# Performance work log

Hardware: AMD Instinct MI355X
Metric: run time of the kernel (lower is better)

## Reference

```python
import jax, jax.numpy as jnp
import numpy as np

# Static config (matches init_kwargs)
B = 1
D = 1024          # model_dim
H = 16            # num_heads
HD = 64           # head_dim
TPF = 256         # tokens_per_frame = latent_height*latent_width
LH, LW = 16, 16
FRAMES = 13
PREFIX = 1
ATTN = 3
CHUNKS = 4
TXT = 226                 # text_length per chunk
SEQ_TXT = CHUNKS * TXT    # 904
VID_LEN = FRAMES * TPF    # 3328
CHUNK_VID = (PREFIX + ATTN) * TPF  # 1024 video tokens per attention chunk
THETA = 10000.0
EPS = 1e-6
SCALE = 1.0 / np.sqrt(HD)
DT, DHE, DW = 16, 24, 24  # 3D rope split of head_dim


def setup_inputs() -> dict:
    key = jax.random.key(0)
    ks = jax.random.split(key, 16)
    def w(k, shape, s=0.02):
        return (jax.random.normal(k, shape) * s).astype(jnp.float32)
    return dict(
        vid_emb=jax.random.normal(ks[0], (B, VID_LEN, D), jnp.float32),
        text_emb=jax.random.normal(ks[1], (B, SEQ_TXT, D), jnp.float32),
        Wq=w(ks[2], (D, D)), bq=jnp.zeros((D,), jnp.float32),
        Wk=w(ks[3], (D, D)), bk=jnp.zeros((D,), jnp.float32),
        Wv=w(ks[4], (D, D)), bv=jnp.zeros((D,), jnp.float32),
        Wo=w(ks[5], (D, D)), bo=jnp.zeros((D,), jnp.float32),
        qn_w=jnp.ones((HD,), jnp.float32), qn_b=jnp.zeros((HD,), jnp.float32),
        kn_w=jnp.ones((HD,), jnp.float32), kn_b=jnp.zeros((HD,), jnp.float32),
        ssm_Win=w(ks[6], (D, D)), ssm_Wout=w(ks[7], (D, D)),
        ssm_gate=jnp.zeros((D,), jnp.float32),
        fg_t=jnp.full((D,), 0.1, jnp.float32), fg_v=jnp.full((D,), 0.1, jnp.float32),
        bg_t=jnp.full((D,), 0.1, jnp.float32), bg_v=jnp.full((D,), 0.1, jnp.float32),
    )


def _layernorm(x, w, b):
    mu = jnp.mean(x, axis=-1, keepdims=True)
    var = jnp.mean((x - mu) ** 2, axis=-1, keepdims=True)
    return (x - mu) * jax.lax.rsqrt(var + EPS) * w + b


def _rope_angles():
    # per-video-token 3D positions within a chunk
    tok = jnp.arange(CHUNK_VID)
    f = (tok // TPF).astype(jnp.float32)
    rem = tok % TPF
    hp = (rem // LW).astype(jnp.float32)
    wp = (rem % LW).astype(jnp.float32)
    def inv(d):
        return THETA ** (-jnp.arange(0, d, 2, dtype=jnp.float32) / d)
    return f[:, None] * inv(DT), hp[:, None] * inv(DHE), wp[:, None] * inv(DW)


def _rot(x, ang):
    half = x.shape[-1] // 2
    c, s = jnp.cos(ang), jnp.sin(ang)
    x1, x2 = x[..., :half], x[..., half:]
    return jnp.concatenate([x1 * c - x2 * s, x1 * s + x2 * c], axis=-1)


def _apply_rope3d(x, angs):
    at, ah, aw = angs
    return jnp.concatenate([
        _rot(x[..., :DT], at),
        _rot(x[..., DT:DT + DHE], ah),
        _rot(x[..., DT + DHE:], aw),
    ], axis=-1)


def _attn_forward(vid_emb, text_emb, Wq, bq, Wk, bk, Wv, bv, Wo, bo, qn_w, qn_b, kn_w, kn_b):
    b = vid_emb.shape[0]
    starts = np.arange(CHUNKS) * ATTN * TPF
    idx = jnp.asarray(starts)[:, None] + jnp.arange(CHUNK_VID)[None, :]  # [C, CHUNK_VID]
    txt_chunks = text_emb.reshape(b, CHUNKS, TXT, D)
    vid_chunks = vid_emb[:, idx]                                          # [b, C, CHUNK_VID, D]
    cur = jnp.concatenate([txt_chunks, vid_chunks], axis=2)               # [b, C, T, D]
    T = TXT + CHUNK_VID
    cur = cur.reshape(b * CHUNKS, T, D)

    def heads(x):
        return x.reshape(b * CHUNKS, T, H, HD).transpose(0, 2, 1, 3)      # [bc, h, t, d]

    q = _layernorm(heads(cur @ Wq + bq), qn_w, qn_b)
    k = _layernorm(heads(cur @ Wk + bk), kn_w, kn_b)
    v = heads(cur @ Wv + bv)

    angs = _rope_angles()
    q = jnp.concatenate([q[:, :, :TXT], _apply_rope3d(q[:, :, TXT:], angs)], axis=2)
    k = jnp.concatenate([k[:, :, :TXT], _apply_rope3d(k[:, :, TXT:], angs)], axis=2)

    scores = jnp.einsum('bhqd,bhkd->bhqk', q, k) * SCALE
    attn = jax.nn.softmax(scores, axis=-1)
    out = jnp.einsum('bhqk,bhkd->bhqd', attn, v)
    out = out.transpose(0, 2, 1, 3).reshape(b * CHUNKS, T, D) @ Wo + bo
    out = out.reshape(b, CHUNKS, T, D)

    text_out = out[:, :, :TXT].reshape(b, SEQ_TXT, D)
    vid_part = out[:, :, TXT:]                                            # [b, C, CHUNK_VID, D]
    vid_acc = jnp.zeros((b, VID_LEN, D), vid_emb.dtype).at[:, idx].add(vid_part)
    cnt = jnp.zeros((b, VID_LEN, 1), vid_emb.dtype).at[:, idx].add(jnp.ones((b, CHUNKS, CHUNK_VID, 1), vid_emb.dtype))
    vid_out = vid_acc / cnt
    return jnp.concatenate([text_out, vid_out], axis=1)


def _ssm(x, Win, Wout, gate_logit):
    # simplified TTT stand-in: gated linear recurrence h_t = g*h_{t-1} + u_t (causal scan)
    g = jax.nn.sigmoid(gate_logit)
    u = x @ Win
    a = jnp.broadcast_to(g, u.shape)
    def comb(c1, c2):
        a1, b1 = c1
        a2, b2 = c2
        return a1 * a2, a2 * b1 + b2
    _, h = jax.lax.associative_scan(comb, (a, u), axis=1)
    return h @ Wout


def _rev_text_chunks(t):
    b = t.shape[0]
    return jnp.flip(t.reshape(b, CHUNKS, TXT, D), axis=1).reshape(b, SEQ_TXT, D)


def _ssm_forward(emb, ssm_Win, ssm_Wout, ssm_gate, fg_t, fg_v, bg_t, bg_v):
    Ttxt = SEQ_TXT
    res = emb
    y = _ssm(emb, ssm_Win, ssm_Wout, ssm_gate)
    emb = res + jnp.concatenate([jnp.tanh(fg_t) * y[:, :Ttxt], jnp.tanh(fg_v) * y[:, Ttxt:]], axis=1)
    res2 = emb
    # multiscene reverse: flip text chunk order and video token order
    rev = jnp.concatenate([_rev_text_chunks(emb[:, :Ttxt]), jnp.flip(emb[:, Ttxt:], axis=1)], axis=1)
    y2 = _ssm(rev, ssm_Win, ssm_Wout, ssm_gate)
    y2 = jnp.concatenate([_rev_text_chunks(y2[:, :Ttxt]), jnp.flip(y2[:, Ttxt:], axis=1)], axis=1)
    return res2 + jnp.concatenate([jnp.tanh(bg_t) * y2[:, :Ttxt], jnp.tanh(bg_v) * y2[:, Ttxt:]], axis=1)


def reference(vid_emb, text_emb, Wq, bq, Wk, bk, Wv, bv, Wo, bo, qn_w, qn_b, kn_w, kn_b,
              ssm_Win, ssm_Wout, ssm_gate, fg_t, fg_v, bg_t, bg_v):
    emb = _attn_forward(vid_emb, text_emb, Wq, bq, Wk, bk, Wv, bv, Wo, bo, qn_w, qn_b, kn_w, kn_b)
    out = _ssm_forward(emb, ssm_Win, ssm_Wout, ssm_gate, fg_t, fg_v, bg_t, bg_v)
    return out[:, SEQ_TXT:], out[:, :SEQ_TXT]
```

## Files before the change

### kernel.cpp

```cpp
#include <hip/hip_runtime.h>
#include <cstdint>

constexpr int Dm       = 1024;
constexpr int Hh       = 16;
constexpr int HD       = 64;
constexpr int CHUNKS   = 4;
constexpr int TXT      = 226;
constexpr int SEQ_TXT  = 904;
constexpr int VID_LEN  = 3328;
constexpr int CHUNK_VID= 1024;
constexpr int Tt       = 1250;
constexpr int Tp       = 1280;
constexpr int M_QKV    = 5000;
constexpr int SEQm     = 4232;
constexpr int STRIDE_V = 768;
constexpr float EPSc   = 1e-6f;
constexpr float SCALEc = 0.125f;
constexpr float OFFS   = 8.0f;
constexpr float C16    = 1.6609640474f;
constexpr float C24    = 1.1073093649f;

constexpr int SEGL2 = 64;
constexpr int HALO  = 64;
constexpr int NSEG2 = (SEQm + SEGL2 - 1) / SEGL2;

typedef __attribute__((ext_vector_type(8))) short bf16x8;
typedef __attribute__((ext_vector_type(4))) float f32x4;

__device__ __forceinline__ ushort f2bf(float x) {
    uint32_t u = __float_as_uint(x);
    u += 0x7FFFu + ((u >> 16) & 1u);
    return (ushort)(u >> 16);
}
__device__ __forceinline__ float bf2f(ushort b) {
    return __uint_as_float(((uint32_t)b) << 16);
}

__device__ __forceinline__ void gload_lds16(const ushort* g, ushort* l) {
    __builtin_amdgcn_global_load_lds(
        (const __attribute__((address_space(1))) unsigned int*)g,
        (__attribute__((address_space(3))) unsigned int*)l, 16, 0, 0);
}

__device__ __forceinline__ int rev_map(int i) {
    if (i < SEQ_TXT) {
        int c = i / TXT, o = i - c * TXT;
        return (CHUNKS - 1 - c) * TXT + o;
    }
    int j = i - SEQ_TXT;
    return SEQ_TXT + (VID_LEN - 1 - j);
}

__global__ __launch_bounds__(256) void prep_all(
    const float* __restrict__ Wq, const float* __restrict__ Wk,
    const float* __restrict__ Wv, const float* __restrict__ Wo,
    const float* __restrict__ Win, const float* __restrict__ Wout,
    const float* __restrict__ vid, const float* __restrict__ txt,
    ushort* __restrict__ WqkvH, ushort* __restrict__ WqkvL,
    ushort* __restrict__ WoH, ushort* __restrict__ WoL,
    ushort* __restrict__ WinH, ushort* __restrict__ WinL,
    ushort* __restrict__ WoutH, ushort* __restrict__ WoutL,
    ushort* __restrict__ chi, ushort* __restrict__ clo) {
    __shared__ float tile[32][33];
    if (blockIdx.z == 6) {
        int base = (blockIdx.y * 32 + blockIdx.x) * 256 + threadIdx.x;
        for (int idx = base; idx < M_QKV * 256; idx += 32 * 32 * 256) {
            int row = idx >> 8, c4 = (idx & 255) * 4;
            int c = row / Tt, t = row - c * Tt;
            float4 x;
            if (t < TXT)
                x = *(const float4*)(txt + (size_t)(c * TXT + t) * Dm + c4);
            else
                x = *(const float4*)(vid + (size_t)(c * STRIDE_V + (t - TXT)) * Dm + c4);
            float v[4] = {x.x, x.y, x.z, x.w};
            ushort4 h, l;
            h.x = f2bf(v[0]); l.x = f2bf(v[0] - bf2f(h.x));
            h.y = f2bf(v[1]); l.y = f2bf(v[1] - bf2f(h.y));
            h.z = f2bf(v[2]); l.z = f2bf(v[2] - bf2f(h.z));
            h.w = f2bf(v[3]); l.w = f2bf(v[3] - bf2f(h.w));
            *(ushort4*)(chi + (size_t)row * Dm + c4) = h;
            *(ushort4*)(clo + (size_t)row * Dm + c4) = l;
        }
        return;
    }
    const float* W; ushort* Thi; ushort* Tlo;
    switch (blockIdx.z) {
        case 0: W = Wq;  Thi = WqkvH;               Tlo = WqkvL;               break;
        case 1: W = Wk;  Thi = WqkvH + 1024*1024;   Tlo = WqkvL + 1024*1024;   break;
        case 2: W = Wv;  Thi = WqkvH + 2*1024*1024; Tlo = WqkvL + 2*1024*1024; break;
        case 3: W = Wo;  Thi = WoH;   Tlo = WoL;   break;
        case 4: W = Win; Thi = WinH;  Tlo = WinL;  break;
        default:W = Wout;Thi = WoutH; Tlo = WoutL; break;
    }
    int k0 = blockIdx.y * 32, n0 = blockIdx.x * 32;
    int j = threadIdx.x & 31, i0 = threadIdx.x >> 5;
#pragma unroll
    for (int i = i0; i < 32; i += 8)
        tile[i][j] = W[(size_t)(k0 + i) * 1024 + n0 + j];
    __syncthreads();
#pragma unroll
    for (int i = i0; i < 32; i += 8) {
        float v = tile[j][i];
        ushort h = f2bf(v);
        size_t o = (size_t)(n0 + i) * 1024 + k0 + j;
        Thi[o] = h;
        Tlo[o] = f2bf(v - bf2f(h));
    }
}

template<int MODE>
__global__ __launch_bounds__(256) void gemm_sk(
    const ushort* __restrict__ Ahi, const ushort* __restrict__ Alo,
    const ushort* __restrict__ Bhi, const ushort* __restrict__ Blo,
    const float* __restrict__ f1, const float* __restrict__ f2,
    const float* __restrict__ f3,
    float* __restrict__ Cf, ushort* __restrict__ u1,
    int M, int N) {
    __shared__ ushort AHL[2][128 * 64];
    __shared__ ushort BHL[2][128 * 64];
    const int tid = threadIdx.x;
    const int w = tid >> 6, lane = tid & 63;
    const int lrow = lane & 15, quad = lane >> 4;
    const int mBase = blockIdx.y * 128, nBase = blockIdx.x * 128;

    const bool isB = (w >= 2);
    const int half = w & 1;
    const ushort* Phi = isB ? Bhi : Ahi;
    const ushort* Plo = isB ? Blo : Alo;
    ushort* st0 = (isB ? BHL[0] : AHL[0]) + half * 4096;
    ushort* st1 = (isB ? BHL[1] : AHL[1]) + half * 4096;
    const int baseR = (isB ? nBase : mBase) + half * 64;
    const int maxr = (isB ? N : M) - 1;
    const int rl8 = lane >> 3;
    const int c = (lane & 7) ^ rl8;
    const ushort* Psel = (c < 4) ? Phi : Plo;
    const ushort* gb[8];
#pragma unroll
    for (int u = 0; u < 8; ++u) {
        int rg = min(baseR + u * 8 + rl8, maxr);
        gb[u] = Psel + (size_t)rg * 1024 + (c & 3) * 8;
    }

    const int mo = (w >> 1) * 64, no = (w & 1) * 64;
    const int p = quad ^ (lrow & 7);
    f32x4 acc[4][4];
#pragma unroll
    for (int i = 0; i < 4; ++i)
#pragma unroll
        for (int j = 0; j < 4; ++j) acc[i][j] = (f32x4){0.f, 0.f, 0.f, 0.f};

    const int kk0 = (MODE == 5) ? blockIdx.z * 512 : 0;
    const int kk1 = (MODE == 5) ? kk0 + 512 : 1024;

#pragma unroll
    for (int u = 0; u < 8; ++u) gload_lds16(gb[u] + kk0, st0 + u * 512);
    asm volatile("s_waitcnt vmcnt(0)" ::: "memory");
    __builtin_amdgcn_s_barrier();

    int it = 0;
    for (int kk = kk0; kk < kk1; kk += 32, ++it) {
        const int b = it & 1;
        ushort* stN = b ? st0 : st1;
        if (kk + 32 < kk1) {
#pragma unroll
            for (int u = 0; u < 8; ++u) gload_lds16(gb[u] + kk + 32, stN + u * 512);
        }

        const ushort* Ab = AHL[b];
        const ushort* Bb = BHL[b];
        bf16x8 ah[4], al[4], bh[4], bl[4];
#pragma unroll
        for (int i = 0; i < 4; ++i) {
            int m = mo + i * 16 + lrow;
            ah[i] = *(const bf16x8*)&Ab[m * 64 + p * 8];
            al[i] = *(const bf16x8*)&Ab[m * 64 + (p ^ 4) * 8];
        }
#pragma unroll
        for (int j = 0; j < 4; ++j) {
            int n = no + j * 16 + lrow;
            bh[j] = *(const bf16x8*)&Bb[n * 64 + p * 8];
            bl[j] = *(const bf16x8*)&Bb[n * 64 + (p ^ 4) * 8];
        }
        __builtin_amdgcn_s_setprio(1);
#pragma unroll
        for (int i = 0; i < 4; ++i)
#pragma unroll
            for (int j = 0; j < 4; ++j) {
                f32x4 a = acc[i][j];
                a = __builtin_amdgcn_mfma_f32_16x16x32_bf16(ah[i], bh[j], a, 0, 0, 0);
                a = __builtin_amdgcn_mfma_f32_16x16x32_bf16(al[i], bh[j], a, 0, 0, 0);
                a = __builtin_amdgcn_mfma_f32_16x16x32_bf16(ah[i], bl[j], a, 0, 0, 0);
                acc[i][j] = a;
            }
        __builtin_amdgcn_s_setprio(0);
        asm volatile("s_waitcnt vmcnt(0)" ::: "memory");
        __builtin_amdgcn_s_barrier();
    }

    const size_t zoff = (MODE == 5) ? (size_t)blockIdx.z * M * N : 0;
#pragma unroll
    for (int i = 0; i < 4; ++i)
#pragma unroll
        for (int j = 0; j < 4; ++j) {
            const int col = nBase + no + j * 16 + lrow;
            float bv = 0.f;
            if constexpr (MODE == 1)
                bv = (col < 1024) ? f1[col]
                   : (col < 2048) ? f2[col - 1024] : f3[col - 2048];
#pragma unroll
            for (int r = 0; r < 4; ++r) {
                const int row = mBase + mo + i * 16 + quad * 4 + r;
                if (row >= M) continue;
                const size_t idx = (size_t)row * N + col;
                const float a = acc[i][j][r];
                if constexpr (MODE == 1) {
                    u1[idx] = f2bf(a + bv);
                } else {
                    Cf[zoff + idx] = a;
                }
            }
        }
}

__global__ __launch_bounds__(512, 2) void gemm_qkv_8ph(
    const ushort* __restrict__ Ahi, const ushort* __restrict__ Alo,
    const ushort* __restrict__ Bhi, const ushort* __restrict__ Blo,
    const float* __restrict__ f1, const float* __restrict__ f2,
    const float* __restrict__ f3, ushort* __restrict__ out) {
    constexpr int Mq  = M_QKV;
    constexpr int Nq  = 3072;
    constexpr int NSL = 32;

    __shared__ __align__(16) ushort ldsq[65536];

    const int tid = threadIdx.x;
    const int w = tid >> 6, lane = tid & 63;
    const int lrow = lane & 15, quad = lane >> 4;
    const int wr = w >> 2, wc = w & 3;
    const int mBase = blockIdx.y * 256, nBase = blockIdx.x * 256;

    const int cA = (tid & 7) ^ ((tid >> 3) & 7);
    const ushort* pA = (cA < 4) ? Ahi : Alo;
    const ushort* pB = (cA < 4) ? Bhi : Blo;
    uint32_t offA[4], offB[4];
#pragma unroll
    for (int q = 0; q < 4; ++q) {
        const int r = q * 64 + (tid >> 3);
        offA[q] = (uint32_t)(min(mBase + r, Mq - 1) * 1024 + (cA & 3) * 8);
        offB[q] = (uint32_t)((nBase + r) * 1024 + (cA & 3) * 8);
    }
    const int ldsW = w * 512;

    const int pH = quad ^ (lrow & 7);
    const int arow = wr * 128 + lrow;
    const int brow = wc * 64 + lrow;

    f32x4 acc[8][4];
#pragma unroll
    for (int i = 0; i < 8; ++i)
#pragma unroll
        for (int j = 0; j < 4; ++j) acc[i][j] = (f32x4){0.f, 0.f, 0.f, 0.f};

#define STAGE_AB(b, s) do { \
        ushort* dA_ = ldsq + (b) * 16384 + ldsW; \
        ushort* dB_ = ldsq + 32768 + (b) * 16384 + ldsW; \
        const uint32_t ko_ = (uint32_t)(s) * 32u; \
        gload_lds16(pA + offA[0] + ko_, dA_); \
        gload_lds16(pA + offA[1] + ko_, dA_ + 4096); \
        gload_lds16(pA + offA[2] + ko_, dA_ + 8192); \
        gload_lds16(pA + offA[3] + ko_, dA_ + 12288); \
        gload_lds16(pB + offB[0] + ko_, dB_); \
        gload_lds16(pB + offB[1] + ko_, dB_ + 4096); \
        gload_lds16(pB + offB[2] + ko_, dB_ + 8192); \
        gload_lds16(pB + offB[3] + ko_, dB_ + 12288); \
    } while (0)

    STAGE_AB(0, 0);
    asm volatile("s_waitcnt vmcnt(0)" ::: "memory");
    __builtin_amdgcn_s_barrier();

#pragma unroll 1
    for (int s = 0; s < NSL; ++s) {
        const int b = s & 1;
        if (s + 1 < NSL) STAGE_AB(1 - b, s + 1);

        const ushort* aB_ = ldsq + b * 16384;
        const ushort* bB_ = ldsq + 32768 + b * 16384;
        bf16x8 ahi[8], alo[8], bhi[4], blo[4];
#pragma unroll
        for (int i = 0; i < 8; ++i) {
            const ushort* rp = aB_ + (arow + i * 16) * 64;
            ahi[i] = *(const bf16x8*)(rp + pH * 8);
            alo[i] = *(const bf16x8*)(rp + (pH ^ 4) * 8);
        }
#pragma unroll
        for (int j = 0; j < 4; ++j) {
            const ushort* rp = bB_ + (brow + j * 16) * 64;
            bhi[j] = *(const bf16x8*)(rp + pH * 8);
            blo[j] = *(const bf16x8*)(rp + (pH ^ 4) * 8);
        }

        __builtin_amdgcn_s_barrier();
        asm volatile("s_waitcnt lgkmcnt(0)" ::: "memory");
        __builtin_amdgcn_s_setprio(1);
#pragma unroll
        for (int i = 0; i < 8; ++i)
#pragma unroll
            for (int j = 0; j < 4; ++j) {
                f32x4 a = acc[i][j];
                a = __builtin_amdgcn_mfma_f32_16x16x32_bf16(ahi[i], bhi[j], a, 0, 0, 0);
                a = __builtin_amdgcn_mfma_f32_16x16x32_bf16(alo[i], bhi[j], a, 0, 0, 0);
                a = __builtin_amdgcn_mfma_f32_16x16x32_bf16(ahi[i], blo[j], a, 0, 0, 0);
                acc[i][j] = a;
            }
        __builtin_amdgcn_s_setprio(0);
        asm volatile("s_waitcnt vmcnt(0)" ::: "memory");
        __builtin_amdgcn_s_barrier();
    }

#undef STAGE_AB

#pragma unroll
    for (int i = 0; i < 8; ++i) {
#pragma unroll
        for (int j = 0; j < 4; ++j) {
            const int col = nBase + wc * 64 + j * 16 + lrow;
            const float bias = (col < 1024) ? f1[col]
                             : (col < 2048) ? f2[col - 1024] : f3[col - 2048];
#pragma unroll
            for (int r = 0; r < 4; ++r) {
                const int row = mBase + wr * 128 + i * 16 + quad * 4 + r;
                if (row < Mq)
                    out[(size_t)row * Nq + col] = f2bf(acc[i][j][r] + bias);
            }
        }
    }
}

__global__ __launch_bounds__(256) void lnrope(
    const ushort* __restrict__ qkvb,
    const float* __restrict__ qn_w, const float* __restrict__ qn_b,
    const float* __restrict__ kn_w, const float* __restrict__ kn_b,
    ushort* __restrict__ qP, ushort* __restrict__ kP, ushort* __restrict__ vT) {
    __shared__ ushort vtile[64][72];
    const int ch = blockIdx.y, c = ch >> 4, h = ch & 15;
    const int t0 = blockIdx.x * 64;
    const int tid = threadIdx.x, w = tid >> 6, lane = tid & 63;

    auto wsum = [](float x) {
#pragma unroll
        for (int o = 32; o; o >>= 1) x += __shfl_xor(x, o);
        return x;
    };

#pragma unroll 1
    for (int it = 0; it < 16; ++it) {
        const int tl = w * 16 + it;
        const int t = t0 + tl;
        ushort qb = 0, kb = 0, vb = 0;
        if (t < Tt) {
            size_t src = (size_t)(c * Tt + t) * 3072 + h * HD + lane;
            float qv = bf2f(qkvb[src]);
            float kv = bf2f(qkvb[src + 1024]);
            float vv = bf2f(qkvb[src + 2048]);

            float qmu = wsum(qv) * (1.f / 64.f);
            float qd  = qv - qmu;
            float qvar = wsum(qd * qd) * (1.f / 64.f);
            float qn = qd * rsqrtf(qvar + EPSc) * qn_w[lane] + qn_b[lane];

            float kmu = wsum(kv) * (1.f / 64.f);
            float kd  = kv - kmu;
            float kvar = wsum(kd * kd) * (1.f / 64.f);
            float kn = kd * rsqrtf(kvar + EPSc) * kn_w[lane] + kn_b[lane];

            if (t >= TXT) {
                int pos = t - TXT;
                int f = pos >> 8, rem2 = pos & 255, hp = rem2 >> 4, wp = rem2 & 15;
                int p, dl; float cc;
                if (lane < 16)      { cc = C16; p = f;  dl = lane; }
                else if (lane < 40) { cc = C24; p = hp; dl = lane - 16; }
                else                { cc = C24; p = wp; dl = lane - 40; }
                int halfd = (lane < 16) ? 8 : 12;
                int i = (dl < halfd) ? dl : dl - halfd;
                float ang = (float)p * exp2f(-(float)i * cc);
                float cs = cosf(ang), sn = sinf(ang);
                int partner = (dl < halfd) ? (lane + halfd) : (lane - halfd);
                float qo = __shfl(qn, partner);
                float ko = __shfl(kn, partner);
                qn = (dl < halfd) ? (qn * cs - qo * sn) : (qo * sn + qn * cs);
                kn = (dl < halfd) ? (kn * cs - ko * sn) : (ko * sn + kn * cs);
            }
            qb = f2bf(qn * SCALEc);
            kb = f2bf(kn);
            vb = f2bf(vv);
        }
        size_t dst = ((size_t)ch * Tp + t) * HD + lane;
        qP[dst] = qb;
        kP[dst] = kb;
        vtile[tl][lane] = vb;
    }
    __syncthreads();
    const int r = tid >> 2, ck = tid & 3;
    ushort* dst = vT + ((size_t)ch * HD + r) * Tp + t0;
    short o1[8], o2[8];
#pragma unroll
    for (int j = 0; j < 8; ++j) {
        o1[j] = (short)vtile[ck * 8 + j][r];
        o2[j] = (short)vtile[(ck + 4) * 8 + j][r];
    }
    *(bf16x8*)(dst + ck * 8)       = *(bf16x8*)o1;
    *(bf16x8*)(dst + (ck + 4) * 8) = *(bf16x8*)o2;
}

__global__ __launch_bounds__(256) void attn_mfma(
    const ushort* __restrict__ qP, const ushort* __restrict__ kP,
    const ushort* __restrict__ vT,
    ushort* __restrict__ ohi, ushort* __restrict__ olo) {
    const int ch = blockIdx.y;
    const int c = ch >> 4, h = ch & 15;
    const int qbase = blockIdx.x * 64;
    const int tid = threadIdx.x, w = tid >> 6, lane = tid & 63;
    const int lrow = lane & 15, quad = lane >> 4;

    __shared__ ushort KT[2][32 * 64];
    __shared__ ushort VTs[2][64 * 32];
    __shared__ ushort PB[4][16][40];

    const ushort* kg = kP + (size_t)ch * Tp * HD;
    const ushort* vg = vT + (size_t)ch * HD * Tp;

    const ushort* kgl = kg + (size_t)(w * 8 + (lane >> 3)) * HD
                           + ((lane & 7) ^ ((lane >> 3) & 7)) * 8;
    const ushort* vgl = vg + (size_t)(w * 16 + (lane >> 2)) * Tp + (lane & 3) * 8;

    const int qr = qbase + w * 16 + lrow;
    const ushort* qgp = qP + ((size_t)ch * Tp + qr) * HD + quad * 8;
    bf16x8 qf0 = *(const bf16x8*)qgp;
    bf16x8 qf1 = *(const bf16x8*)(qgp + 32);

    f32x4 accO[4];
#pragma unroll
    for (int dt = 0; dt < 4; ++dt) accO[dt] = (f32x4){0.f, 0.f, 0.f, 0.f};
    float lacc[4] = {0.f, 0.f, 0.f, 0.f};

    gload_lds16(kgl, &KT[0][w * 512]);
    gload_lds16(vgl, &VTs[0][w * 512]);

    const int NSTEP = Tp / 32;
    for (int s = 0; s < NSTEP; ++s) {
        const int b = s & 1;
        __syncthreads();
        if (s + 1 < NSTEP) {
            int kb = (s + 1) * 32;
            gload_lds16(kgl + (size_t)kb * HD, &KT[1 - b][w * 512]);
            gload_lds16(vgl + kb, &VTs[1 - b][w * 512]);
        }

        const int sw = lrow & 7;
        const ushort* r0 = &KT[b][lrow * 64];
        const ushort* r1 = &KT[b][(16 + lrow) * 64];
        bf16x8 k00 = *(const bf16x8*)(r0 + (quad ^ sw) * 8);
        bf16x8 k01 = *(const bf16x8*)(r0 + ((4 + quad) ^ sw) * 8);
        bf16x8 k10 = *(const bf16x8*)(r1 + (quad ^ sw) * 8);
        bf16x8 k11 = *(const bf16x8*)(r1 + ((4 + quad) ^ sw) * 8);
        f32x4 s0 = (f32x4){0.f, 0.f, 0.f, 0.f}, s1 = s0;
        s0 = __builtin_amdgcn_mfma_f32_16x16x32_bf16(qf0, k00, s0, 0, 0, 0);
        s0 = __builtin_amdgcn_mfma_f32_16x16x32_bf16(qf1, k01, s0, 0, 0, 0);
        s1 = __builtin_amdgcn_mfma_f32_16x16x32_bf16(qf0, k10, s1, 0, 0, 0);
        s1 = __builtin_amdgcn_mfma_f32_16x16x32_bf16(qf1, k11, s1, 0, 0, 0);

#pragma unroll
        for (int r = 0; r < 4; ++r) {
            float p0 = __expf(s0[r] - OFFS);
            float p1 = __expf(s1[r] - OFFS);
            lacc[r] += p0 + p1;
            int row = quad * 4 + r;
            PB[w][row][lrow]      = f2bf(p0);
            PB[w][row][16 + lrow] = f2bf(p1);
        }

        bf16x8 pf = *(const bf16x8*)&PB[w][lrow][quad * 8];
#pragma unroll
        for (int dt = 0; dt < 4; ++dt) {
            bf16x8 vf = *(const bf16x8*)&VTs[b][(dt * 16 + lrow) * 32 + quad * 8];
            accO[dt] = __builtin_amdgcn_mfma_f32_16x16x32_bf16(pf, vf, accO[dt], 0, 0, 0);
        }
    }

    float il[4];
#pragma unroll
    for (int r = 0; r < 4; ++r) {
        float l = lacc[r];
        l += __shfl_xor(l, 1);
        l += __shfl_xor(l, 2);
        l += __shfl_xor(l, 4);
        l += __shfl_xor(l, 8);
        l -= (float)(Tp - Tt) * __expf(-OFFS);
        il[r] = 1.f / l;
    }
#pragma unroll
    for (int dt = 0; dt < 4; ++dt)
#pragma unroll
        for (int r = 0; r < 4; ++r) {
            int qrow = qbase + w * 16 + quad * 4 + r;
            if (qrow < Tt) {
                float val = accO[dt][r] * il[r];
                size_t o = (size_t)(c * Tt + qrow) * Dm + h * HD + dt * 16 + lrow;
                ushort hv = f2bf(val);
                ohi[o] = hv;
                olo[o] = f2bf(val - bf2f(hv));
            }
        }
}

__global__ __launch_bounds__(256) void reduce_scatter(
    const float* __restrict__ P0, const float* __restrict__ bo,
    ushort* __restrict__ ehi, ushort* __restrict__ elo) {
    const float* P1 = P0 + (size_t)M_QKV * Dm;
    int idx = blockIdx.x * 256 + threadIdx.x;
    int row = idx >> 8, c4 = (idx & 255) * 4;
    float sx, sy, sz, sw;
    if (row < SEQ_TXT) {
        int c = row / TXT, t = row - c * TXT;
        size_t o = (size_t)(c * Tt + t) * Dm + c4;
        float4 a = *(const float4*)(P0 + o);
        float4 b = *(const float4*)(P1 + o);
        sx = a.x + b.x; sy = a.y + b.y; sz = a.z + b.z; sw = a.w + b.w;
    } else {
        int p = row - SEQ_TXT;
        sx = sy = sz = sw = 0.f; int cnt = 0;
#pragma unroll
        for (int c = 0; c < CHUNKS; ++c) {
            int off = p - c * STRIDE_V;
            if (off >= 0 && off < CHUNK_VID) {
                size_t o = (size_t)(c * Tt + TXT + off) * Dm + c4;
                float4 a = *(const float4*)(P0 + o);
                float4 b = *(const float4*)(P1 + o);
                sx += a.x + b.x; sy += a.y + b.y;
                sz += a.z + b.z; sw += a.w + b.w;
                ++cnt;
            }
        }
        float inv = 1.f / (float)cnt;
        sx *= inv; sy *= inv; sz *= inv; sw *= inv;
    }
    float4 b4 = *(const float4*)(bo + c4);
    float v[4] = {sx + b4.x, sy + b4.y, sz + b4.z, sw + b4.w};
    ushort4 h, l;
    h.x = f2bf(v[0]); l.x = f2bf(v[0] - bf2f(h.x));
    h.y = f2bf(v[1]); l.y = f2bf(v[1] - bf2f(h.y));
    h.z = f2bf(v[2]); l.z = f2bf(v[2] - bf2f(h.z));
    h.w = f2bf(v[3]); l.w = f2bf(v[3] - bf2f(h.w));
    *(ushort4*)(ehi + (size_t)row * Dm + c4) = h;
    *(ushort4*)(elo + (size_t)row * Dm + c4) = l;
}

__global__ __launch_bounds__(256) void scan_halo(
    const float* __restrict__ P0, const float* __restrict__ gate,
    ushort* __restrict__ hhi, ushort* __restrict__ hlo, int perm) {
    const float* P1 = P0 + (size_t)SEQm * Dm;
    int ch = blockIdx.x * 256 + threadIdx.x;
    int seg = blockIdx.y;
    float g = 1.f / (1.f + expf(-gate[ch]));
    int tw0 = seg * SEGL2;
    int tw1 = min(SEQm, tw0 + SEGL2);
    int t0 = max(0, tw0 - HALO);
    float hv = 0.f;
    for (int t = t0; t < tw0; ++t) {
        int rt = perm ? rev_map(t) : t;
        size_t o = (size_t)rt * Dm + ch;
        hv = fmaf(g, hv, P0[o] + P1[o]);
    }
    for (int t = tw0; t < tw1; ++t) {
        int rt = perm ? rev_map(t) : t;
        size_t o = (size_t)rt * Dm + ch;
        hv = fmaf(g, hv, P0[o] + P1[o]);
        ushort h = f2bf(hv);
        hhi[o] = h;
        hlo[o] = f2bf(hv - bf2f(h));
    }
}

__global__ __launch_bounds__(256) void reduce_c1(
    const float* __restrict__ P0,
    const ushort* __restrict__ ehi, const ushort* __restrict__ elo,
    const float* __restrict__ fg_t, const float* __restrict__ fg_v,
    float* __restrict__ emb2, ushort* __restrict__ e2hi, ushort* __restrict__ e2lo) {
    const float* P1 = P0 + (size_t)SEQm * Dm;
    int idx = blockIdx.x * 256 + threadIdx.x;
    int row = idx >> 8, c4 = (idx & 255) * 4;
    const float* fg = (row < SEQ_TXT) ? fg_t : fg_v;
    size_t o = (size_t)row * Dm + c4;
    float4 a = *(const float4*)(P0 + o);
    float4 b = *(const float4*)(P1 + o);
    ushort4 eh = *(const ushort4*)(ehi + o);
    ushort4 el = *(const ushort4*)(elo + o);
    float v[4];
    v[0] = (bf2f(eh.x) + bf2f(el.x)) + tanhf(fg[c4 + 0]) * (a.x + b.x);
    v[1] = (bf2f(eh.y) + bf2f(el.y)) + tanhf(fg[c4 + 1]) * (a.y + b.y);
    v[2] = (bf2f(eh.z) + bf2f(el.z)) + tanhf(fg[c4 + 2]) * (a.z + b.z);
    v[3] = (bf2f(eh.w) + bf2f(el.w)) + tanhf(fg[c4 + 3]) * (a.w + b.w);
    *(float4*)(emb2 + o) = make_float4(v[0], v[1], v[2], v[3]);
    ushort4 h, l;
    h.x = f2bf(v[0]); l.x = f2bf(v[0] - bf2f(h.x));
    h.y = f2bf(v[1]); l.y = f2bf(v[1] - bf2f(h.y));
    h.z = f2bf(v[2]); l.z = f2bf(v[2] - bf2f(h.z));
    h.w = f2bf(v[3]); l.w = f2bf(v[3] - bf2f(h.w));
    *(ushort4*)(e2hi + o) = h;
    *(ushort4*)(e2lo + o) = l;
}

__global__ __launch_bounds__(256) void reduce_fin(
    const float* __restrict__ P0, const float* __restrict__ emb2,
    const float* __restrict__ bg_t, const float* __restrict__ bg_v,
    float* __restrict__ outp) {
    const float* P1 = P0 + (size_t)SEQm * Dm;
    int idx = blockIdx.x * 256 + threadIdx.x;
    int row = idx >> 8, c4 = (idx & 255) * 4;
    const float* bg = (row < SEQ_TXT) ? bg_t : bg_v;
    int drow = (row >= SEQ_TXT) ? (row - SEQ_TXT) : (VID_LEN + row);
    size_t o = (size_t)row * Dm + c4;
    float4 a = *(const float4*)(P0 + o);
    float4 b = *(const float4*)(P1 + o);
    float4 e = *(const float4*)(emb2 + o);
    float4 r = make_float4(e.x + tanhf(bg[c4 + 0]) * (a.x + b.x),
                           e.y + tanhf(bg[c4 + 1]) * (a.y + b.y),
                           e.z + tanhf(bg[c4 + 2]) * (a.z + b.z),
                           e.w + tanhf(bg[c4 + 3]) * (a.w + b.w));
    *(float4*)(outp + (size_t)drow * Dm + c4) = r;
}

extern "C" void kernel_launch(void* const* d_in, const int* in_sizes, int n_in,
                              void* d_out, int out_size, void* d_ws, size_t ws_size,
                              hipStream_t stream) {
    const float* vid_emb = (const float*)d_in[0];
    const float* text_emb= (const float*)d_in[1];
    const float* Wq = (const float*)d_in[2];  const float* bq = (const float*)d_in[3];
    const float* Wk = (const float*)d_in[4];  const float* bk = (const float*)d_in[5];
    const float* Wv = (const float*)d_in[6];  const float* bv = (const float*)d_in[7];
    const float* Wo = (const float*)d_in[8];  const float* bo = (const float*)d_in[9];
    const float* qn_w = (const float*)d_in[10]; const float* qn_b = (const float*)d_in[11];
    const float* kn_w = (const float*)d_in[12]; const float* kn_b = (const float*)d_in[13];
    const float* Win  = (const float*)d_in[14]; const float* Wout = (const float*)d_in[15];
    const float* gate = (const float*)d_in[16];
    const float* fg_t = (const float*)d_in[17]; const float* fg_v = (const float*)d_in[18];
    const float* bg_t = (const float*)d_in[19]; const float* bg_v = (const float*)d_in[20];

    char* W8 = (char*)d_ws;
    if (ws_size < 128647168u) return;
    ushort* WqkvH = (ushort*)(W8 + 0);
    ushort* WqkvL = (ushort*)(W8 + 6291456);
    ushort* WoH   = (ushort*)(W8 + 12582912);
    ushort* WoL   = (ushort*)(W8 + 14680064);
    ushort* WinH  = (ushort*)(W8 + 16777216);
    ushort* WinL  = (ushort*)(W8 + 18874368);
    ushort* WoutH = (ushort*)(W8 + 20971520);
    ushort* WoutL = (ushort*)(W8 + 23068672);
    ushort* qkvb  = (ushort*)(W8 + 25165824);
    ushort* curH  = (ushort*)(W8 + 55885824);
    ushort* curL  = (ushort*)(W8 + 66125824);
    ushort* qPl   = (ushort*)(W8 + 76365824);
    ushort* kPl   = (ushort*)(W8 + 86851584);
    ushort* vTl   = (ushort*)(W8 + 97337344);
    ushort* aoutH = (ushort*)(W8 + 25165824);
    ushort* aoutL = (ushort*)(W8 + 35405824);
    float*  PWo   = (float*) (W8 + 76365824);
    ushort* embH  = (ushort*)(W8 + 45645824);
    ushort* embL  = (ushort*)(W8 + 54312960);
    float*  PW    = (float*) (W8 + 76365824);
    ushort* hbufH = (ushort*)(W8 + 25165824);
    ushort* hbufL = (ushort*)(W8 + 33832960);
    float*  emb2  = (float*) (W8 + 111034368);
    ushort* e2H   = (ushort*)(W8 + 25165824);
    ushort* e2L   = (ushort*)(W8 + 33832960);
    ushort* hbuf2H= (ushort*)(W8 + 45645824);
    ushort* hbuf2L= (ushort*)(W8 + 54312960);
    float*  outp  = (float*)d_out;

    prep_all<<<dim3(32, 32, 7), 256, 0, stream>>>(
        Wq, Wk, Wv, Wo, Win, Wout, vid_emb, text_emb,
        WqkvH, WqkvL, WoH, WoL, WinH, WinL, WoutH, WoutL, curH, curL);

    gemm_qkv_8ph<<<dim3(12, 20), 512, 0, stream>>>(
        curH, curL, WqkvH, WqkvL, bq, bk, bv, qkvb);

    lnrope<<<dim3(Tp / 64, 64), 256, 0, stream>>>(qkvb, qn_w, qn_b, kn_w, kn_b,
                                                  qPl, kPl, vTl);

    attn_mfma<<<dim3(Tp / 64, 64), 256, 0, stream>>>(qPl, kPl, vTl, aoutH, aoutL);

    gemm_sk<5><<<dim3(8, 40, 2), 256, 0, stream>>>(
        aoutH, aoutL, WoH, WoL, nullptr, nullptr, nullptr, PWo, nullptr,
        M_QKV, 1024);
    reduce_scatter<<<SEQm, 256, 0, stream>>>(PWo, bo, embH, embL);

    dim3 gsq(8, 34, 2);
    dim3 gscan(Dm / 256, NSEG2);

    gemm_sk<5><<<gsq, 256, 0, stream>>>(
        embH, embL, WinH, WinL, nullptr, nullptr, nullptr, PW, nullptr,
        SEQm, 1024);
    scan_halo<<<gscan, 256, 0, stream>>>(PW, gate, hbufH, hbufL, 0);
    gemm_sk<5><<<gsq, 256, 0, stream>>>(
        hbufH, hbufL, WoutH, WoutL, nullptr, nullptr, nullptr, PW, nullptr,
        SEQm, 1024);
    reduce_c1<<<SEQm, 256, 0, stream>>>(PW, embH, embL, fg_t, fg_v,
                                        emb2, e2H, e2L);

    gemm_sk<5><<<gsq, 256, 0, stream>>>(
        e2H, e2L, WinH, WinL, nullptr, nullptr, nullptr, PW, nullptr,
        SEQm, 1024);
    scan_halo<<<gscan, 256, 0, stream>>>(PW, gate, hbuf2H, hbuf2L, 1);
    gemm_sk<5><<<gsq, 256, 0, stream>>>(
        hbuf2H, hbuf2L, WoutH, WoutL, nullptr, nullptr, nullptr, PW, nullptr,
        SEQm, 1024);
    reduce_fin<<<SEQm, 256, 0, stream>>>(PW, emb2, bg_t, bg_v, outp);
}
```

Baseline: 647.2 us.

## Replace split-K GEMM with full-K 128x64 tile GEMM and drop partial sums

Result: no change. 647.7 us (median of 2 runs) (+0.1%).

```diff
diff --git a/kernel.cpp b/kernel.cpp
--- a/kernel.cpp
+++ b/kernel.cpp
@@ -108,84 +108,77 @@
     }
 }
 
-template<int MODE>
-__global__ __launch_bounds__(256) void gemm_sk(
+__global__ __launch_bounds__(256) void gemm_fk(
     const ushort* __restrict__ Ahi, const ushort* __restrict__ Alo,
     const ushort* __restrict__ Bhi, const ushort* __restrict__ Blo,
-    const float* __restrict__ f1, const float* __restrict__ f2,
-    const float* __restrict__ f3,
-    float* __restrict__ Cf, ushort* __restrict__ u1,
-    int M, int N) {
+    float* __restrict__ Cf, int M, int N) {
     __shared__ ushort AHL[2][128 * 64];
-    __shared__ ushort BHL[2][128 * 64];
+    __shared__ ushort BHL[2][64 * 64];
     const int tid = threadIdx.x;
     const int w = tid >> 6, lane = tid & 63;
     const int lrow = lane & 15, quad = lane >> 4;
-    const int mBase = blockIdx.y * 128, nBase = blockIdx.x * 128;
-
-    const bool isB = (w >= 2);
-    const int half = w & 1;
-    const ushort* Phi = isB ? Bhi : Ahi;
-    const ushort* Plo = isB ? Blo : Alo;
-    ushort* st0 = (isB ? BHL[0] : AHL[0]) + half * 4096;
-    ushort* st1 = (isB ? BHL[1] : AHL[1]) + half * 4096;
-    const int baseR = (isB ? nBase : mBase) + half * 64;
-    const int maxr = (isB ? N : M) - 1;
-    const int rl8 = lane >> 3;
-    const int c = (lane & 7) ^ rl8;
-    const ushort* Psel = (c < 4) ? Phi : Plo;
-    const ushort* gb[8];
-#pragma unroll
-    for (int u = 0; u < 8; ++u) {
-        int rg = min(baseR + u * 8 + rl8, maxr);
-        gb[u] = Psel + (size_t)rg * 1024 + (c & 3) * 8;
-    }
-
-    const int mo = (w >> 1) * 64, no = (w & 1) * 64;
+    const int mBase = blockIdx.y * 128, nBase = blockIdx.x * 64;
+
+    const int srow = tid >> 3;
+    const int cch  = (tid & 7) ^ (srow & 7);
+    const ushort* PA = (cch < 4) ? Ahi : Alo;
+    const ushort* PB = (cch < 4) ? Bhi : Blo;
+    uint32_t gA[4], gB[2];
+#pragma unroll
+    for (int q = 0; q < 4; ++q)
+        gA[q] = (uint32_t)(min(mBase + q * 32 + srow, M - 1) * 1024 + (cch & 3) * 8);
+#pragma unroll
+    for (int q = 0; q < 2; ++q)
+        gB[q] = (uint32_t)((nBase + q * 32 + srow) * 1024 + (cch & 3) * 8);
+    const int ldsW = w * 512;
+
+    const int wm = w >> 1, wn = w & 1;
     const int p = quad ^ (lrow & 7);
-    f32x4 acc[4][4];
+    const int arow = wm * 64 + lrow;
+    const int brow = wn * 32 + lrow;
+
+    f32x4 acc[4][2];
 #pragma unroll
     for (int i = 0; i < 4; ++i)
 #pragma unroll
-        for (int j = 0; j < 4; ++j) acc[i][j] = (f32x4){0.f, 0.f, 0.f, 0.f};
-
-    const int kk0 = (MODE == 5) ? blockIdx.z * 512 : 0;
-    const int kk1 = (MODE == 5) ? kk0 + 512 : 1024;
-
-#pragma unroll
-    for (int u = 0; u < 8; ++u) gload_lds16(gb[u] + kk0, st0 + u * 512);
+        for (int j = 0; j < 2; ++j) acc[i][j] = (f32x4){0.f, 0.f, 0.f, 0.f};
+
+#define STAGE_FK(buf, kk) do { \
+        gload_lds16(PA + gA[0] + (kk), &AHL[buf][0 * 2048 + ldsW]); \
+        gload_lds16(PA + gA[1] + (kk), &AHL[buf][1 * 2048 + ldsW]); \
+        gload_lds16(PA + gA[2] + (kk), &AHL[buf][2 * 2048 + ldsW]); \
+        gload_lds16(PA + gA[3] + (kk), &AHL[buf][3 * 2048 + ldsW]); \
+        gload_lds16(PB + gB[0] + (kk), &BHL[buf][0 * 2048 + ldsW]); \
+        gload_lds16(PB + gB[1] + (kk), &BHL[buf][1 * 2048 + ldsW]); \
+    } while (0)
+
+    STAGE_FK(0, 0);
     asm volatile("s_waitcnt vmcnt(0)" ::: "memory");
     __builtin_amdgcn_s_barrier();
 
     int it = 0;
-    for (int kk = kk0; kk < kk1; kk += 32, ++it) {
+    for (int kk = 0; kk < 1024; kk += 32, ++it) {
         const int b = it & 1;
-        ushort* stN = b ? st0 : st1;
-        if (kk + 32 < kk1) {
-#pragma unroll
-            for (int u = 0; u < 8; ++u) gload_lds16(gb[u] + kk + 32, stN + u * 512);
-        }
-
-        const ushort* Ab = AHL[b];
-        const ushort* Bb = BHL[b];
-        bf16x8 ah[4], al[4], bh[4], bl[4];
+        if (kk + 32 < 1024) STAGE_FK(1 - b, kk + 32);
+
+        bf16x8 ah[4], al[4], bh[2], bl[2];
 #pragma unroll
         for (int i = 0; i < 4; ++i) {
-            int m = mo + i * 16 + lrow;
-            ah[i] = *(const bf16x8*)&Ab[m * 64 + p * 8];
-            al[i] = *(const bf16x8*)&Ab[m * 64 + (p ^ 4) * 8];
-        }
-#pragma unroll
-        for (int j = 0; j < 4; ++j) {
-            int n = no + j * 16 + lrow;
-            bh[j] = *(const bf16x8*)&Bb[n * 64 + p * 8];
-            bl[j] = *(const bf16x8*)&Bb[n * 64 + (p ^ 4) * 8];
+            const ushort* rp = &AHL[b][(arow + i * 16) * 64];
+            ah[i] = *(const bf16x8*)(rp + p * 8);
+            al[i] = *(const bf16x8*)(rp + (p ^ 4) * 8);
+        }
+#pragma unroll
+        for (int j = 0; j < 2; ++j) {
+            const ushort* rp = &BHL[b][(brow + j * 16) * 64];
+            bh[j] = *(const bf16x8*)(rp + p * 8);
+            bl[j] = *(const bf16x8*)(rp + (p ^ 4) * 8);
         }
         __builtin_amdgcn_s_setprio(1);
 #pragma unroll
         for (int i = 0; i < 4; ++i)
 #pragma unroll
-            for (int j = 0; j < 4; ++j) {
+            for (int j = 0; j < 2; ++j) {
                 f32x4 a = acc[i][j];
                 a = __builtin_amdgcn_mfma_f32_16x16x32_bf16(ah[i], bh[j], a, 0, 0, 0);
                 a = __builtin_amdgcn_mfma_f32_16x16x32_bf16(al[i], bh[j], a, 0, 0, 0);
@@ -196,28 +189,17 @@
         asm volatile("s_waitcnt vmcnt(0)" ::: "memory");
         __builtin_amdgcn_s_barrier();
     }
-
-    const size_t zoff = (MODE == 5) ? (size_t)blockIdx.z * M * N : 0;
+#undef STAGE_FK
+
 #pragma unroll
     for (int i = 0; i < 4; ++i)
 #pragma unroll
-        for (int j = 0; j < 4; ++j) {
-            const int col = nBase + no + j * 16 + lrow;
-            float bv = 0.f;
-            if constexpr (MODE == 1)
-                bv = (col < 1024) ? f1[col]
-                   : (col < 2048) ? f2[col - 1024] : f3[col - 2048];
+        for (int j = 0; j < 2; ++j) {
+            const int col = nBase + wn * 32 + j * 16 + lrow;
 #pragma unroll
             for (int r = 0; r < 4; ++r) {
-                const int row = mBase + mo + i * 16 + quad * 4 + r;
-                if (row >= M) continue;
-                const size_t idx = (size_t)row * N + col;
-                const float a = acc[i][j][r];
-                if constexpr (MODE == 1) {
-                    u1[idx] = f2bf(a + bv);
-                } else {
-                    Cf[zoff + idx] = a;
-                }
+                const int row = mBase + wm * 64 + i * 16 + quad * 4 + r;
+                if (row < M) Cf[(size_t)row * N + col] = acc[i][j][r];
             }
         }
 }
@@ -517,7 +499,6 @@
 __global__ __launch_bounds__(256) void reduce_scatter(
     const float* __restrict__ P0, const float* __restrict__ bo,
     ushort* __restrict__ ehi, ushort* __restrict__ elo) {
-    const float* P1 = P0 + (size_t)M_QKV * Dm;
     int idx = blockIdx.x * 256 + threadIdx.x;
     int row = idx >> 8, c4 = (idx & 255) * 4;
     float sx, sy, sz, sw;
@@ -525,8 +506,7 @@
         int c = row / TXT, t = row - c * TXT;
         size_t o = (size_t)(c * Tt + t) * Dm + c4;
         float4 a = *(const float4*)(P0 + o);
-        float4 b = *(const float4*)(P1 + o);
-        sx = a.x + b.x; sy = a.y + b.y; sz = a.z + b.z; sw = a.w + b.w;
+        sx = a.x; sy = a.y; sz = a.z; sw = a.w;
     } else {
         int p = row - SEQ_TXT;
         sx = sy = sz = sw = 0.f; int cnt = 0;
@@ -536,9 +516,7 @@
             if (off >= 0 && off < CHUNK_VID) {
                 size_t o = (size_t)(c * Tt + TXT + off) * Dm + c4;
                 float4 a = *(const float4*)(P0 + o);
-                float4 b = *(const float4*)(P1 + o);
-                sx += a.x + b.x; sy += a.y + b.y;
-                sz += a.z + b.z; sw += a.w + b.w;
+                sx += a.x; sy += a.y; sz += a.z; sw += a.w;
                 ++cnt;
             }
         }
@@ -559,7 +537,6 @@
 __global__ __launch_bounds__(256) void scan_halo(
     const float* __restrict__ P0, const float* __restrict__ gate,
     ushort* __restrict__ hhi, ushort* __restrict__ hlo, int perm) {
-    const float* P1 = P0 + (size_t)SEQm * Dm;
     int ch = blockIdx.x * 256 + threadIdx.x;
     int seg = blockIdx.y;
     float g = 1.f / (1.f + expf(-gate[ch]));
@@ -569,13 +546,12 @@
     float hv = 0.f;
     for (int t = t0; t < tw0; ++t) {
         int rt = perm ? rev_map(t) : t;
-        size_t o = (size_t)rt * Dm + ch;
-        hv = fmaf(g, hv, P0[o] + P1[o]);
+        hv = fmaf(g, hv, P0[(size_t)rt * Dm + ch]);
     }
     for (int t = tw0; t < tw1; ++t) {
         int rt = perm ? rev_map(t) : t;
         size_t o = (size_t)rt * Dm + ch;
-        hv = fmaf(g, hv, P0[o] + P1[o]);
+        hv = fmaf(g, hv, P0[o]);
         ushort h = f2bf(hv);
         hhi[o] = h;
         hlo[o] = f2bf(hv - bf2f(h));
@@ -587,20 +563,18 @@
     const ushort* __restrict__ ehi, const ushort* __restrict__ elo,
     const float* __restrict__ fg_t, const float* __restrict__ fg_v,
     float* __restrict__ emb2, ushort* __restrict__ e2hi, ushort* __restrict__ e2lo) {
-    const float* P1 = P0 + (size_t)SEQm * Dm;
     int idx = blockIdx.x * 256 + threadIdx.x;
     int row = idx >> 8, c4 = (idx & 255) * 4;
     const float* fg = (row < SEQ_TXT) ? fg_t : fg_v;
     size_t o = (size_t)row * Dm + c4;
     float4 a = *(const float4*)(P0 + o);
-    float4 b = *(const float4*)(P1 + o);
     ushort4 eh = *(const ushort4*)(ehi + o);
     ushort4 el = *(const ushort4*)(elo + o);
     float v[4];
-    v[0] = (bf2f(eh.x) + bf2f(el.x)) + tanhf(fg[c4 + 0]) * (a.x + b.x);
-    v[1] = (bf2f(eh.y) + bf2f(el.y)) + tanhf(fg[c4 + 1]) * (a.y + b.y);
-    v[2] = (bf2f(eh.z) + bf2f(el.z)) + tanhf(fg[c4 + 2]) * (a.z + b.z);
-    v[3] = (bf2f(eh.w) + bf2f(el.w)) + tanhf(fg[c4 + 3]) * (a.w + b.w);
+    v[0] = (bf2f(eh.x) + bf2f(el.x)) + tanhf(fg[c4 + 0]) * a.x;
+    v[1] = (bf2f(eh.y) + bf2f(el.y)) + tanhf(fg[c4 + 1]) * a.y;
+    v[2] = (bf2f(eh.z) + bf2f(el.z)) + tanhf(fg[c4 + 2]) * a.z;
+    v[3] = (bf2f(eh.w) + bf2f(el.w)) + tanhf(fg[c4 + 3]) * a.w;
     *(float4*)(emb2 + o) = make_float4(v[0], v[1], v[2], v[3]);
     ushort4 h, l;
     h.x = f2bf(v[0]); l.x = f2bf(v[0] - bf2f(h.x));
@@ -615,19 +589,17 @@
     const float* __restrict__ P0, const float* __restrict__ emb2,
     const float* __restrict__ bg_t, const float* __restrict__ bg_v,
     float* __restrict__ outp) {
-    const float* P1 = P0 + (size_t)SEQm * Dm;
     int idx = blockIdx.x * 256 + threadIdx.x;
     int row = idx >> 8, c4 = (idx & 255) * 4;
     const float* bg = (row < SEQ_TXT) ? bg_t : bg_v;
     int drow = (row >= SEQ_TXT) ? (row - SEQ_TXT) : (VID_LEN + row);
     size_t o = (size_t)row * Dm + c4;
     float4 a = *(const float4*)(P0 + o);
-    float4 b = *(const float4*)(P1 + o);
     float4 e = *(const float4*)(emb2 + o);
-    float4 r = make_float4(e.x + tanhf(bg[c4 + 0]) * (a.x + b.x),
-                           e.y + tanhf(bg[c4 + 1]) * (a.y + b.y),
-                           e.z + tanhf(bg[c4 + 2]) * (a.z + b.z),
-                           e.w + tanhf(bg[c4 + 3]) * (a.w + b.w));
+    float4 r = make_float4(e.x + tanhf(bg[c4 + 0]) * a.x,
+                           e.y + tanhf(bg[c4 + 1]) * a.y,
+                           e.z + tanhf(bg[c4 + 2]) * a.z,
+                           e.w + tanhf(bg[c4 + 3]) * a.w);
     *(float4*)(outp + (size_t)drow * Dm + c4) = r;
 }
 
@@ -690,30 +662,21 @@
 
     attn_mfma<<<dim3(Tp / 64, 64), 256, 0, stream>>>(qPl, kPl, vTl, aoutH, aoutL);
 
-    gemm_sk<5><<<dim3(8, 40, 2), 256, 0, stream>>>(
-        aoutH, aoutL, WoH, WoL, nullptr, nullptr, nullptr, PWo, nullptr,
-        M_QKV, 1024);
+    gemm_fk<<<dim3(16, 40), 256, 0, stream>>>(
+        aoutH, aoutL, WoH, WoL, PWo, M_QKV, 1024);
     reduce_scatter<<<SEQm, 256, 0, stream>>>(PWo, bo, embH, embL);
 
-    dim3 gsq(8, 34, 2);
+    dim3 gfk(16, 34);
     dim3 gscan(Dm / 256, NSEG2);
 
-    gemm_sk<5><<<gsq, 256, 0, stream>>>(
-        embH, embL, WinH, WinL, nullptr, nullptr, nullptr, PW, nullptr,
-        SEQm, 1024);
+    gemm_fk<<<gfk, 256, 0, stream>>>(embH, embL, WinH, WinL, PW, SEQm, 1024);
     scan_halo<<<gscan, 256, 0, stream>>>(PW, gate, hbufH, hbufL, 0);
-    gemm_sk<5><<<gsq, 256, 0, stream>>>(
-        hbufH, hbufL, WoutH, WoutL, nullptr, nullptr, nullptr, PW, nullptr,
-        SEQm, 1024);
+    gemm_fk<<<gfk, 256, 0, stream>>>(hbufH, hbufL, WoutH, WoutL, PW, SEQm, 1024);
     reduce_c1<<<SEQm, 256, 0, stream>>>(PW, embH, embL, fg_t, fg_v,
                                         emb2, e2H, e2L);
 
-    gemm_sk<5><<<gsq, 256, 0, stream>>>(
-        e2H, e2L, WinH, WinL, nullptr, nullptr, nullptr, PW, nullptr,
-        SEQm, 1024);
+    gemm_fk<<<gfk, 256, 0, stream>>>(e2H, e2L, WinH, WinL, PW, SEQm, 1024);
     scan_halo<<<gscan, 256, 0, stream>>>(PW, gate, hbuf2H, hbuf2L, 1);
-    gemm_sk<5><<<gsq, 256, 0, stream>>>(
-        hbuf2H, hbuf2L, WoutH, WoutL, nullptr, nullptr, nullptr, PW, nullptr,
-        SEQm, 1024);
+    gemm_fk<<<gfk, 256, 0, stream>>>(hbuf2H, hbuf2L, WoutH, WoutL, PW, SEQm, 1024);
     reduce_fin<<<SEQm, 256, 0, stream>>>(PW, emb2, bg_t, bg_v, outp);
 }
```
